# Optimization experiments

Measured on AMD Instinct MI355X. Metric: run time of the kernel, lower is better.

Reference implementation:

```python
import jax, jax.numpy as jnp
import numpy as np

NEG_SLOPE = 0.2  # PyG GATConv default leaky_relu negative_slope


def gat_conv(x, edge_index, W, att_src, att_dst, bias, heads, out_ch):
    """PyG GATConv (add_self_loops=False, concat=True, dropout disabled)."""
    N = x.shape[0]
    src, dst = edge_index[0], edge_index[1]
    h = (x @ W).reshape(N, heads, out_ch)               # [N,H,C]
    a_src = jnp.einsum('nhc,hc->nh', h, att_src)        # [N,H]
    a_dst = jnp.einsum('nhc,hc->nh', h, att_dst)        # [N,H]
    e = jax.nn.leaky_relu(a_src[src] + a_dst[dst], NEG_SLOPE)  # [E,H]
    # segment softmax over edges grouped by destination node
    e_max = jax.ops.segment_max(e, dst, num_segments=N)  # [N,H]
    e_exp = jnp.exp(e - e_max[dst])
    denom = jax.ops.segment_sum(e_exp, dst, num_segments=N)
    alpha = e_exp / (denom[dst] + 1e-16)                 # [E,H]
    msg = h[src] * alpha[:, :, None]                     # [E,H,C]
    out = jax.ops.segment_sum(msg, dst, num_segments=N)  # [N,H,C]
    return out.reshape(N, heads * out_ch) + bias


def setup_inputs() -> dict:
    key = jax.random.key(0)
    ks = jax.random.split(key, 10)
    N, E, F_IN, H, C1, OUT = 50000, 1600000, 256, 8, 8, 64
    s = 0.1
    return {
        'x': jax.random.normal(ks[0], (N, F_IN), jnp.float32),
        'edge_index': jax.random.randint(ks[1], (2, E), 0, N, jnp.int64),
        'W1': jax.random.normal(ks[2], (F_IN, H * C1), jnp.float32) * s,
        'att_src1': jax.random.normal(ks[3], (H, C1), jnp.float32) * s,
        'att_dst1': jax.random.normal(ks[4], (H, C1), jnp.float32) * s,
        'bias1': jax.random.normal(ks[5], (H * C1,), jnp.float32) * s,
        'W2': jax.random.normal(ks[6], (H * C1, OUT), jnp.float32) * s,
        'att_src2': jax.random.normal(ks[7], (1, OUT), jnp.float32) * s,
        'att_dst2': jax.random.normal(ks[8], (1, OUT), jnp.float32) * s,
        'bias2': jax.random.normal(ks[9], (OUT,), jnp.float32) * s,
    }


def reference(x, edge_index, W1, att_src1, att_dst1, bias1, W2, att_src2, att_dst2, bias2):
    # GAT.forward, eval mode with disable_dropout=True (no dropout, no loss)
    h = gat_conv(x, edge_index, W1, att_src1, att_dst1, bias1, heads=8, out_ch=8)
    h = jax.nn.elu(h)
    h = gat_conv(h, edge_index, W2, att_src2, att_dst2, bias2, heads=1, out_ch=64)
    return jax.nn.log_softmax(h, axis=1)
```

## Files before the change

### kernel.cpp

```cpp
#include <hip/hip_runtime.h>
#include <math.h>

#define LRELU 0.2f
#define BSH 7
#define BSZ (1 << BSH)
#define CH 8192
#define ECH 2048
#define GB 6

typedef __attribute__((ext_vector_type(8))) short bf16x8;
typedef __attribute__((ext_vector_type(4))) float f32x4;

static __device__ __forceinline__ float bf2f(unsigned int u16) {
    union { unsigned int i; float f; } c; c.i = u16 << 16; return c.f;
}
static __device__ __forceinline__ unsigned short f2bf(float f) {
    union { float f; unsigned int i; } c; c.f = f;
    unsigned int x = c.i;
    return (unsigned short)((x + 0x7fffu + ((x >> 16) & 1u)) >> 16);
}


__global__ __launch_bounds__(256) void k_bcount(const int* __restrict__ dst, int E,
                                                int NB, int* __restrict__ bcnt) {
    __shared__ int cnt[512];
    int t = threadIdx.x;
    for (int b = t; b < 512; b += 256) cnt[b] = 0;
    __syncthreads();
    int e0 = blockIdx.x * CH;
    int e1 = e0 + CH; if (e1 > E) e1 = E;
    for (int i = e0 + t; i < e1; i += 256) atomicAdd(&cnt[dst[i] >> BSH], 1);
    __syncthreads();
    for (int b = t; b < NB; b += 256) {
        int c = cnt[b];
        if (c) atomicAdd(&bcnt[b], c);
    }
}

__global__ __launch_bounds__(64) void k_bscan(const int* __restrict__ bcnt, int NB,
                                              int* __restrict__ boff,
                                              int* __restrict__ bcur) {
    int lane = threadIdx.x;
    int run = 0;
    for (int base = 0; base < NB; base += 64) {
        int v = (base + lane < NB) ? bcnt[base + lane] : 0;
        int inc = v;
#pragma unroll
        for (int off = 1; off < 64; off <<= 1) {
            int t = __shfl_up(inc, off, 64);
            if (lane >= off) inc += t;
        }
        if (base + lane < NB) {
            int e = run + inc - v;
            boff[base + lane] = e;
            bcur[base + lane] = e;
        }
        run += __shfl(inc, 63, 64);
    }
    if (lane == 0) boff[NB] = run;
}

__global__ __launch_bounds__(256) void k_binscat1(const int* __restrict__ src,
                                                  const int* __restrict__ dst,
                                                  int E, int NB,
                                                  int* __restrict__ bcur,
                                                  unsigned* __restrict__ pairs) {
    __shared__ int cnt[512];
    __shared__ int lds_d[CH];
    int t = threadIdx.x;
    int e0 = blockIdx.x * CH;
    int e1 = e0 + CH; if (e1 > E) e1 = E;
    int n = e1 - e0;
    for (int b = t; b < 512; b += 256) cnt[b] = 0;
    __syncthreads();
    for (int i = t; i < n; i += 256) {
        int d = dst[e0 + i];
        lds_d[i] = d;
        atomicAdd(&cnt[d >> BSH], 1);
    }
    __syncthreads();
    for (int b = t; b < NB; b += 256) {
        int c = cnt[b];
        cnt[b] = c ? atomicAdd(&bcur[b], c) : 0;
    }
    __syncthreads();
    for (int i = t; i < n; i += 256) {
        int d = lds_d[i];
        int p = atomicAdd(&cnt[d >> BSH], 1);
        pairs[p] = ((unsigned)src[e0 + i] << BSH) | (unsigned)(d & (BSZ - 1));
    }
}

__global__ __launch_bounds__(256) void k_bucket(const int* __restrict__ boff,
                                                const unsigned* __restrict__ pairs,
                                                int N, int* __restrict__ rowptr,
                                                int* __restrict__ col) {
    __shared__ int cnt[BSZ];
    __shared__ int cur[BSZ];
    int t = threadIdx.x;
    int b = blockIdx.x;
    int dlo = b << BSH;
    int dhi = dlo + BSZ; if (dhi > N) dhi = N;
    int nd = dhi - dlo;
    int jb = boff[b], je = boff[b + 1];
    if (t < BSZ) cnt[t] = 0;
    __syncthreads();
    for (int j = jb + t; j < je; j += 256) atomicAdd(&cnt[pairs[j] & (BSZ - 1)], 1);
    __syncthreads();
    if (t < 64) {
        int v0 = cnt[t], v1 = cnt[64 + t];
        int i0 = v0;
#pragma unroll
        for (int off = 1; off < 64; off <<= 1) {
            int q = __shfl_up(i0, off, 64);
            if (t >= off) i0 += q;
        }
        int tot0 = __shfl(i0, 63, 64);
        int i1 = v1;
#pragma unroll
        for (int off = 1; off < 64; off <<= 1) {
            int q = __shfl_up(i1, off, 64);
            if (t >= off) i1 += q;
        }
        int e0x = jb + i0 - v0;
        int e1x = jb + tot0 + i1 - v1;
        cur[t] = e0x;
        cur[64 + t] = e1x;
        if (t < nd) rowptr[dlo + t] = e0x;
        if (64 + t < nd) rowptr[dlo + 64 + t] = e1x;
        if (t == 0 && dhi == N) rowptr[N] = je;
    }
    __syncthreads();
    for (int j = jb + t; j < je; j += 256) {
        unsigned pk = pairs[j];
        int p = atomicAdd(&cur[pk & (BSZ - 1)], 1);
        col[p] = (int)(pk >> BSH);
    }
}

__global__ __launch_bounds__(256) void k_cvtW(const float* __restrict__ W1,
                                              const float* __restrict__ W2,
                                              unsigned short* __restrict__ Wt1,
                                              unsigned short* __restrict__ Wt2,
                                              float* __restrict__ s1,
                                              float* __restrict__ s2,
                                              unsigned short* __restrict__ h1b,
                                              unsigned short* __restrict__ gb,
                                              int N) {
    int idx = blockIdx.x * 256 + threadIdx.x;
    if (idx < 16384) {
        int n = idx >> 8, k = idx & 255;
        Wt1[idx] = f2bf(W1[k * 64 + n]);
    } else if (idx < 16384 + 4096) {
        int j = idx - 16384;
        int n = j >> 6, k = j & 63;
        Wt2[j] = f2bf(W2[k * 64 + n]);
    } else if (idx < 20488) {
        s1[(size_t)N * 8 + (idx - 20480)] = -1e30f;
    } else if (idx == 20488) {
        s2[N] = -1e30f;
    } else if (idx >= 20496 && idx < 20560) {
        h1b[(size_t)N * 64 + (idx - 20496)] = 0;
    } else if (idx >= 20560 && idx < 20624) {
        gb[(size_t)N * 64 + (idx - 20560)] = 0;
    }
}

__global__ __launch_bounds__(256) void k_gemm1m(const float* __restrict__ X,
                                                const unsigned short* __restrict__ Wt,
                                                const float* __restrict__ atts,
                                                const float* __restrict__ attd,
                                                int N, unsigned short* __restrict__ Hb,
                                                float* __restrict__ asrc,
                                                float* __restrict__ adst) {
    __shared__ short Xl[64 * 256];
    int t = threadIdx.x, l = t & 63, w = t >> 6;
    int rblk = blockIdx.x * 64;

    int half = l >> 5;
    int c8 = (l & 31) * 8;
#pragma unroll
    for (int i = 0; i < 8; ++i) {
        int rl = w * 16 + i * 2 + half;
        int row = rblk + rl;
        float4 x0 = {0.f, 0.f, 0.f, 0.f}, x1 = {0.f, 0.f, 0.f, 0.f};
        if (row < N) {
            x0 = *reinterpret_cast<const float4*>(X + (size_t)row * 256 + c8);
            x1 = *reinterpret_cast<const float4*>(X + (size_t)row * 256 + c8 + 4);
        }
        bf16x8 p;
        p[0] = (short)f2bf(x0.x); p[1] = (short)f2bf(x0.y);
        p[2] = (short)f2bf(x0.z); p[3] = (short)f2bf(x0.w);
        p[4] = (short)f2bf(x1.x); p[5] = (short)f2bf(x1.y);
        p[6] = (short)f2bf(x1.z); p[7] = (short)f2bf(x1.w);
        int g = (l & 31) ^ (rl & 7);
        *reinterpret_cast<bf16x8*>(&Xl[rl * 256 + g * 8]) = p;
    }

    int m = l & 15, quad = l >> 4;
    int rl = w * 16 + m;
    f32x4 acc0 = {0.f, 0.f, 0.f, 0.f}, acc1 = acc0, acc2 = acc0, acc3 = acc0;
#pragma unroll
    for (int tt = 0; tt < 8; ++tt) {
        int g = (tt * 4 + quad) ^ (m & 7);
        bf16x8 a = *reinterpret_cast<const bf16x8*>(&Xl[rl * 256 + g * 8]);
        int kk = tt * 32 + quad * 8;
        bf16x8 b0 = *reinterpret_cast<const bf16x8*>(&Wt[(0 * 16 + m) * 256 + kk]);
        bf16x8 b1 = *reinterpret_cast<const bf16x8*>(&Wt[(1 * 16 + m) * 256 + kk]);
        bf16x8 b2 = *reinterpret_cast<const bf16x8*>(&Wt[(2 * 16 + m) * 256 + kk]);
        bf16x8 b3 = *reinterpret_cast<const bf16x8*>(&Wt[(3 * 16 + m) * 256 + kk]);
        acc0 = __builtin_amdgcn_mfma_f32_16x16x32_bf16(a, b0, acc0, 0, 0, 0);
        acc1 = __builtin_amdgcn_mfma_f32_16x16x32_bf16(a, b1, acc1, 0, 0, 0);
        acc2 = __builtin_amdgcn_mfma_f32_16x16x32_bf16(a, b2, acc2, 0, 0, 0);
        acc3 = __builtin_amdgcn_mfma_f32_16x16x32_bf16(a, b3, acc3, 0, 0, 0);
    }

    int r0 = rblk + w * 16;
    f32x4 accs[4] = {acc0, acc1, acc2, acc3};
#pragma unroll
    for (int nt = 0; nt < 4; ++nt) {
        int cn = nt * 16 + m;
        float av_s = atts[cn], av_d = attd[cn];
#pragma unroll
        for (int r = 0; r < 4; ++r) {
            int row = r0 + quad * 4 + r;
            float hv = accs[nt][r];
            if (row < N) Hb[(size_t)row * 64 + cn] = f2bf(hv);
            float vs = hv * av_s, vd = hv * av_d;
            vs += __shfl_xor(vs, 1, 64); vs += __shfl_xor(vs, 2, 64); vs += __shfl_xor(vs, 4, 64);
            vd += __shfl_xor(vd, 1, 64); vd += __shfl_xor(vd, 2, 64); vd += __shfl_xor(vd, 4, 64);
            if ((m & 7) == 0 && row < N) {
                int head = cn >> 3;
                asrc[row * 8 + head] = vs;
                adst[row * 8 + head] = vd;
            }
        }
    }
}

__global__ __launch_bounds__(256) void k_gemm2m(const unsigned short* __restrict__ Xb,
                                                const unsigned short* __restrict__ Wt,
                                                const float* __restrict__ atts,
                                                const float* __restrict__ attd,
                                                int N, unsigned short* __restrict__ Gb,
                                                float* __restrict__ asrc,
                                                float* __restrict__ adst) {
    int t = threadIdx.x, l = t & 63, w = t >> 6;
    int rblk = blockIdx.x * 64;
    int m = l & 15, quad = l >> 4;
    int row = rblk + w * 16 + m;
    int rowc = (row < N) ? row : 0;

    f32x4 acc0 = {0.f, 0.f, 0.f, 0.f}, acc1 = acc0, acc2 = acc0, acc3 = acc0;
#pragma unroll
    for (int tt = 0; tt < 2; ++tt) {
        int kk = tt * 32 + quad * 8;
        bf16x8 a = *reinterpret_cast<const bf16x8*>(&Xb[(size_t)rowc * 64 + kk]);
        bf16x8 b0 = *reinterpret_cast<const bf16x8*>(&Wt[(0 * 16 + m) * 64 + kk]);
        bf16x8 b1 = *reinterpret_cast<const bf16x8*>(&Wt[(1 * 16 + m) * 64 + kk]);
        bf16x8 b2 = *reinterpret_cast<const bf16x8*>(&Wt[(2 * 16 + m) * 64 + kk]);
        bf16x8 b3 = *reinterpret_cast<const bf16x8*>(&Wt[(3 * 16 + m) * 64 + kk]);
        acc0 = __builtin_amdgcn_mfma_f32_16x16x32_bf16(a, b0, acc0, 0, 0, 0);
        acc1 = __builtin_amdgcn_mfma_f32_16x16x32_bf16(a, b1, acc1, 0, 0, 0);
        acc2 = __builtin_amdgcn_mfma_f32_16x16x32_bf16(a, b2, acc2, 0, 0, 0);
        acc3 = __builtin_amdgcn_mfma_f32_16x16x32_bf16(a, b3, acc3, 0, 0, 0);
    }

    int r0 = rblk + w * 16;
    f32x4 accs[4] = {acc0, acc1, acc2, acc3};
#pragma unroll
    for (int r = 0; r < 4; ++r) {
        int orow = r0 + quad * 4 + r;
        float vs = 0.f, vd = 0.f;
#pragma unroll
        for (int nt = 0; nt < 4; ++nt) {
            int cn = nt * 16 + m;
            float hv = accs[nt][r];
            if (orow < N) Gb[(size_t)orow * 64 + cn] = f2bf(hv);
            vs = fmaf(hv, atts[cn], vs);
            vd = fmaf(hv, attd[cn], vd);
        }
#pragma unroll
        for (int off = 1; off < 16; off <<= 1) {
            vs += __shfl_xor(vs, off, 64);
            vd += __shfl_xor(vd, off, 64);
        }
        if (m == 0 && orow < N) { asrc[orow] = vs; adst[orow] = vd; }
    }
}


__global__ __launch_bounds__(256) void k_gather1(const int* __restrict__ rowptr,
                                                 const int* __restrict__ col,
                                                 const uint4* __restrict__ Hb8,
                                                 const float* __restrict__ asrc,
                                                 const float* __restrict__ adst,
                                                 const float* __restrict__ bias,
                                                 int N,
                                                 unsigned short* __restrict__ outb) {
    __shared__ int colS[ECH];
    int t = threadIdx.x;
    int gid = t >> 3, sub = t & 7;
    int d0 = blockIdx.x * 32;
    int dend = d0 + 32; if (dend > N) dend = N;
    int d = d0 + gid;
    int dok = (d < dend);
    int dc = dok ? d : d0;
    int jb = rowptr[dc];
    int je = rowptr[dc + 1];
    if (!dok) { jb = 0; je = 0; }
    float adv = dok ? adst[dc * 8 + sub] : 0.f;
    int ebeg = rowptr[d0];
    int eend = rowptr[dend];

    float acc[8] = {0.f, 0.f, 0.f, 0.f, 0.f, 0.f, 0.f, 0.f};
    float denom = 0.f;
    for (int cb = ebeg; cb < eend; cb += ECH) {
        int ce = cb + ECH; if (ce > eend) ce = eend;
        int n = ce - cb;
        __syncthreads();
        for (int i = t; i < n; i += 256) colS[i] = col[cb + i];
        __syncthreads();
        int lo = (jb > cb) ? jb : cb;
        int hi = (je < ce) ? je : ce;
        for (int u = lo; u < hi; u += GB) {
            int s6[GB];
#pragma unroll
            for (int q = 0; q < GB; ++q) {
                int uu = u + q;
                s6[q] = (uu < hi) ? colS[uu - cb] : N;
            }
            float as6[GB];
#pragma unroll
            for (int q = 0; q < GB; ++q) as6[q] = asrc[s6[q] * 8 + sub];
            uint4 hv6[GB];
#pragma unroll
            for (int q = 0; q < GB; ++q) hv6[q] = Hb8[(size_t)s6[q] * 8 + sub];
            __builtin_amdgcn_sched_barrier(0);
#pragma unroll
            for (int q = 0; q < GB; ++q) {
                float e = as6[q] + adv;
                e = (e > 0.f) ? e : LRELU * e;
                float wgt = __expf(e);
                uint4 hv = hv6[q];
                denom += wgt;
                acc[0] = fmaf(wgt, bf2f(hv.x & 0xffffu), acc[0]);
                acc[1] = fmaf(wgt, bf2f(hv.x >> 16), acc[1]);
                acc[2] = fmaf(wgt, bf2f(hv.y & 0xffffu), acc[2]);
                acc[3] = fmaf(wgt, bf2f(hv.y >> 16), acc[3]);
                acc[4] = fmaf(wgt, bf2f(hv.z & 0xffffu), acc[4]);
                acc[5] = fmaf(wgt, bf2f(hv.z >> 16), acc[5]);
                acc[6] = fmaf(wgt, bf2f(hv.w & 0xffffu), acc[6]);
                acc[7] = fmaf(wgt, bf2f(hv.w >> 16), acc[7]);
            }
        }
    }
    if (dok) {
        float invd = 1.f / (denom + 1e-16f);
        unsigned short pk[8];
#pragma unroll
        for (int c = 0; c < 8; ++c) {
            float v = fmaf(acc[c], invd, bias[sub * 8 + c]);
            v = (v > 0.f) ? v : expm1f(v);
            pk[c] = f2bf(v);
        }
        uint4 pv;
        pv.x = (unsigned)pk[0] | ((unsigned)pk[1] << 16);
        pv.y = (unsigned)pk[2] | ((unsigned)pk[3] << 16);
        pv.z = (unsigned)pk[4] | ((unsigned)pk[5] << 16);
        pv.w = (unsigned)pk[6] | ((unsigned)pk[7] << 16);
        *reinterpret_cast<uint4*>(&outb[(size_t)d * 64 + sub * 8]) = pv;
    }
}

__global__ __launch_bounds__(256) void k_gather2(const int* __restrict__ rowptr,
                                                 const int* __restrict__ col,
                                                 const uint4* __restrict__ Gb8,
                                                 const float* __restrict__ asrc,
                                                 const float* __restrict__ adst,
                                                 const float* __restrict__ bias,
                                                 int N,
                                                 float* __restrict__ out) {
    __shared__ int colS[ECH];
    int t = threadIdx.x;
    int gid = t >> 3, sub = t & 7;
    int d0 = blockIdx.x * 32;
    int dend = d0 + 32; if (dend > N) dend = N;
    int d = d0 + gid;
    int dok = (d < dend);
    int dc = dok ? d : d0;
    int jb = rowptr[dc];
    int je = rowptr[dc + 1];
    if (!dok) { jb = 0; je = 0; }
    float adv = dok ? adst[dc] : 0.f;
    int ebeg = rowptr[d0];
    int eend = rowptr[dend];

    float acc[8] = {0.f, 0.f, 0.f, 0.f, 0.f, 0.f, 0.f, 0.f};
    float denom = 0.f;
    for (int cb = ebeg; cb < eend; cb += ECH) {
        int ce = cb + ECH; if (ce > eend) ce = eend;
        int n = ce - cb;
        __syncthreads();
        for (int i = t; i < n; i += 256) colS[i] = col[cb + i];
        __syncthreads();
        int lo = (jb > cb) ? jb : cb;
        int hi = (je < ce) ? je : ce;
        for (int u = lo; u < hi; u += GB) {
            int s6[GB];
#pragma unroll
            for (int q = 0; q < GB; ++q) {
                int uu = u + q;
                s6[q] = (uu < hi) ? colS[uu - cb] : N;
            }
            float as6[GB];
#pragma unroll
            for (int q = 0; q < GB; ++q) as6[q] = asrc[s6[q]];
            uint4 hv6[GB];
#pragma unroll
            for (int q = 0; q < GB; ++q) hv6[q] = Gb8[(size_t)s6[q] * 8 + sub];
            __builtin_amdgcn_sched_barrier(0);
#pragma unroll
            for (int q = 0; q < GB; ++q) {
                float e = as6[q] + adv;
                e = (e > 0.f) ? e : LRELU * e;
                float wgt = __expf(e);
                uint4 hv = hv6[q];
                denom += wgt;
                acc[0] = fmaf(wgt, bf2f(hv.x & 0xffffu), acc[0]);
                acc[1] = fmaf(wgt, bf2f(hv.x >> 16), acc[1]);
                acc[2] = fmaf(wgt, bf2f(hv.y & 0xffffu), acc[2]);
                acc[3] = fmaf(wgt, bf2f(hv.y >> 16), acc[3]);
                acc[4] = fmaf(wgt, bf2f(hv.z & 0xffffu), acc[4]);
                acc[5] = fmaf(wgt, bf2f(hv.z >> 16), acc[5]);
                acc[6] = fmaf(wgt, bf2f(hv.w & 0xffffu), acc[6]);
                acc[7] = fmaf(wgt, bf2f(hv.w >> 16), acc[7]);
            }
        }
    }
    float invd = 1.f / (denom + 1e-16f);
    float v[8];
#pragma unroll
    for (int c = 0; c < 8; ++c) v[c] = fmaf(acc[c], invd, bias[sub * 8 + c]);
    float m = v[0];
#pragma unroll
    for (int c = 1; c < 8; ++c) m = fmaxf(m, v[c]);
    m = fmaxf(m, __shfl_xor(m, 1, 64));
    m = fmaxf(m, __shfl_xor(m, 2, 64));
    m = fmaxf(m, __shfl_xor(m, 4, 64));
    float se = 0.f;
#pragma unroll
    for (int c = 0; c < 8; ++c) se += __expf(v[c] - m);
    se += __shfl_xor(se, 1, 64);
    se += __shfl_xor(se, 2, 64);
    se += __shfl_xor(se, 4, 64);
    float ls = m + __logf(se);
    if (dok) {
        float4 o0, o1;
        o0.x = v[0] - ls; o0.y = v[1] - ls; o0.z = v[2] - ls; o0.w = v[3] - ls;
        o1.x = v[4] - ls; o1.y = v[5] - ls; o1.z = v[6] - ls; o1.w = v[7] - ls;
        *reinterpret_cast<float4*>(&out[(size_t)d * 64 + sub * 8]) = o0;
        *reinterpret_cast<float4*>(&out[(size_t)d * 64 + sub * 8 + 4]) = o1;
    }
}


extern "C" void kernel_launch(void* const* d_in, const int* in_sizes, int n_in,
                              void* d_out, int out_size, void* d_ws, size_t ws_size,
                              hipStream_t stream) {
    const float* x   = (const float*)d_in[0];
    const int*   ei  = (const int*)d_in[1];
    const float* W1  = (const float*)d_in[2];
    const float* as1 = (const float*)d_in[3];
    const float* ad1 = (const float*)d_in[4];
    const float* b1  = (const float*)d_in[5];
    const float* W2  = (const float*)d_in[6];
    const float* as2 = (const float*)d_in[7];
    const float* ad2 = (const float*)d_in[8];
    const float* b2  = (const float*)d_in[9];
    float* out = (float*)d_out;

    const int N = in_sizes[0] / 256;
    const int E = in_sizes[1] / 2;
    const int* src = ei;
    const int* dst = ei + E;
    const int NB = (N + BSZ - 1) >> BSH;
    const int nchunk = (E + CH - 1) / CH;

    char* ws = (char*)d_ws;
    size_t off = 0;
    auto alloc = [&](size_t bytes) -> void* {
        void* p = ws + off;
        off = (off + bytes + 255) & ~(size_t)255;
        return p;
    };
    int*      bcnt   = (int*)alloc((size_t)NB * 4);
    int*      boff   = (int*)alloc((size_t)(NB + 1) * 4);
    int*      bcur   = (int*)alloc((size_t)NB * 4);
    int*      rowptr = (int*)alloc((size_t)(N + 1) * 4);
    int*      col    = (int*)alloc((size_t)E * 4);
    unsigned* pairs  = (unsigned*)alloc((size_t)E * 4);
    unsigned short* wt1 = (unsigned short*)alloc(64 * 256 * 2);
    unsigned short* wt2 = (unsigned short*)alloc(64 * 64 * 2);
    unsigned short* h1b = (unsigned short*)alloc((size_t)(N + 1) * 64 * 2);
    float* a_s1   = (float*)alloc(((size_t)N * 8 + 8) * 4);
    float* a_d1   = (float*)alloc((size_t)N * 8 * 4);
    unsigned short* h2b = (unsigned short*)alloc((size_t)N * 64 * 2);
    unsigned short* gb  = (unsigned short*)alloc((size_t)(N + 1) * 64 * 2);
    float* a_s2   = (float*)alloc((size_t)(N + 1) * 4);
    float* a_d2   = (float*)alloc((size_t)N * 4);
    (void)ws_size; (void)n_in; (void)out_size;

    k_cvtW<<<81, 256, 0, stream>>>(W1, W2, wt1, wt2, a_s1, a_s2, h1b, gb, N);

    hipMemsetAsync(bcnt, 0, (size_t)NB * 4, stream);
    k_bcount<<<nchunk, 256, 0, stream>>>(dst, E, NB, bcnt);
    k_bscan<<<1, 64, 0, stream>>>(bcnt, NB, boff, bcur);
    k_binscat1<<<nchunk, 256, 0, stream>>>(src, dst, E, NB, bcur, pairs);
    k_bucket<<<NB, 256, 0, stream>>>(boff, pairs, N, rowptr, col);

    int gblk = (N + 63) / 64;
    k_gemm1m<<<gblk, 256, 0, stream>>>(x, wt1, as1, ad1, N, h1b, a_s1, a_d1);

    int gather_blocks = (N + 31) / 32;
    k_gather1<<<gather_blocks, 256, 0, stream>>>(rowptr, col, (const uint4*)h1b,
                                                 a_s1, a_d1, b1, N, h2b);

    k_gemm2m<<<gblk, 256, 0, stream>>>(h2b, wt2, as2, ad2, N, gb, a_s2, a_d2);

    k_gather2<<<gather_blocks, 256, 0, stream>>>(rowptr, col, (const uint4*)gb,
                                                 a_s2, a_d2, b2, N, out);
}
```

Before: 249.9 us.

## Fuse layer-2 GEMM into layer-1 gather and merge prep kernels

Layer-2's linear projection now runs inside the layer-1 gather kernel. Each block stages its 32 ELU outputs in swizzled LDS and runs MFMA against the bf16 W2 to write the layer-2 features directly. The attention logits are computed from precomputed W2·att vectors in fp32 before bf16 rounding. The weight conversion and edge-bucket counting kernels are merged into one launch, and the gather batch size rises from 6 to 8 edges. This removes the h2b round trip and one launch, at the cost of more registers and a block-wide barrier in the gather kernel.

```diff
diff --git a/kernel.cpp b/kernel.cpp
--- a/kernel.cpp
+++ b/kernel.cpp
@@ -6,7 +6,7 @@
 #define BSZ (1 << BSH)
 #define CH 8192
 #define ECH 2048
-#define GB 6
+#define GB 8
 
 typedef __attribute__((ext_vector_type(8))) short bf16x8;
 typedef __attribute__((ext_vector_type(4))) float f32x4;
@@ -21,19 +21,64 @@
 }
 
 
-__global__ __launch_bounds__(256) void k_bcount(const int* __restrict__ dst, int E,
-                                                int NB, int* __restrict__ bcnt) {
+__global__ __launch_bounds__(256) void k_prep(const int* __restrict__ dst, int E,
+                                              int NB, int* __restrict__ bcnt,
+                                              const float* __restrict__ W1,
+                                              const float* __restrict__ W2,
+                                              const float* __restrict__ as2in,
+                                              const float* __restrict__ ad2in,
+                                              unsigned short* __restrict__ Wt1,
+                                              unsigned short* __restrict__ Wt2,
+                                              float* __restrict__ s1,
+                                              float* __restrict__ s2,
+                                              unsigned short* __restrict__ h1b,
+                                              unsigned short* __restrict__ gb,
+                                              float* __restrict__ w2s,
+                                              float* __restrict__ w2d,
+                                              int N, int nchunk) {
     __shared__ int cnt[512];
     int t = threadIdx.x;
-    for (int b = t; b < 512; b += 256) cnt[b] = 0;
-    __syncthreads();
-    int e0 = blockIdx.x * CH;
-    int e1 = e0 + CH; if (e1 > E) e1 = E;
-    for (int i = e0 + t; i < e1; i += 256) atomicAdd(&cnt[dst[i] >> BSH], 1);
-    __syncthreads();
-    for (int b = t; b < NB; b += 256) {
-        int c = cnt[b];
-        if (c) atomicAdd(&bcnt[b], c);
+    if ((int)blockIdx.x < nchunk) {
+        for (int b = t; b < 512; b += 256) cnt[b] = 0;
+        __syncthreads();
+        int e0 = blockIdx.x * CH;
+        int e1 = e0 + CH; if (e1 > E) e1 = E;
+        for (int i = e0 + t; i < e1; i += 256) atomicAdd(&cnt[dst[i] >> BSH], 1);
+        __syncthreads();
+        for (int b = t; b < NB; b += 256) {
+            int c = cnt[b];
+            if (c) atomicAdd(&bcnt[b], c);
+        }
+        return;
+    }
+    int idx = ((int)blockIdx.x - nchunk) * 256 + t;
+    if (idx < 16384) {
+        int n = idx >> 8, k = idx & 255;
+        Wt1[idx] = f2bf(W1[k * 64 + n]);
+    } else if (idx < 16384 + 4096) {
+        int j = idx - 16384;
+        int n = j >> 6, k = j & 63;
+        Wt2[j] = f2bf(W2[k * 64 + n]);
+    } else if (idx >= 20480 && idx < 20488) {
+        s1[(size_t)N * 8 + (idx - 20480)] = -1e30f;
+    } else if (idx == 20488) {
+        s2[N] = -1e30f;
+    } else if (idx >= 20496 && idx < 20560) {
+        h1b[(size_t)N * 64 + (idx - 20496)] = 0;
+    } else if (idx >= 20560 && idx < 20624) {
+        gb[(size_t)N * 64 + (idx - 20560)] = 0;
+    } else if (idx >= 20624 && idx < 20688) {
+        int c = idx - 20624;
+        float s = 0.f;
+#pragma unroll
+        for (int n = 0; n < 64; ++n) s += W2[c * 64 + n] * as2in[n];
+        w2s[c] = s;
+    } else if (idx >= 20688 && idx < 20752) {
+        int c = idx - 20688;
+        float s = 0.f;
+#pragma unroll
+        for (int n = 0; n < 64; ++n) s += W2[c * 64 + n] * ad2in[n];
+        w2d[c] = s;
     }
 }
 
@@ -138,34 +183,6 @@
     }
 }
 
-__global__ __launch_bounds__(256) void k_cvtW(const float* __restrict__ W1,
-                                              const float* __restrict__ W2,
-                                              unsigned short* __restrict__ Wt1,
-                                              unsigned short* __restrict__ Wt2,
-                                              float* __restrict__ s1,
-                                              float* __restrict__ s2,
-                                              unsigned short* __restrict__ h1b,
-                                              unsigned short* __restrict__ gb,
-                                              int N) {
-    int idx = blockIdx.x * 256 + threadIdx.x;
-    if (idx < 16384) {
-        int n = idx >> 8, k = idx & 255;
-        Wt1[idx] = f2bf(W1[k * 64 + n]);
-    } else if (idx < 16384 + 4096) {
-        int j = idx - 16384;
-        int n = j >> 6, k = j & 63;
-        Wt2[j] = f2bf(W2[k * 64 + n]);
-    } else if (idx < 20488) {
-        s1[(size_t)N * 8 + (idx - 20480)] = -1e30f;
-    } else if (idx == 20488) {
-        s2[N] = -1e30f;
-    } else if (idx >= 20496 && idx < 20560) {
-        h1b[(size_t)N * 64 + (idx - 20496)] = 0;
-    } else if (idx >= 20560 && idx < 20624) {
-        gb[(size_t)N * 64 + (idx - 20560)] = 0;
-    }
-}
-
 __global__ __launch_bounds__(256) void k_gemm1m(const float* __restrict__ X,
                                                 const unsigned short* __restrict__ Wt,
                                                 const float* __restrict__ atts,
@@ -238,67 +255,22 @@
     }
 }
 
-__global__ __launch_bounds__(256) void k_gemm2m(const unsigned short* __restrict__ Xb,
-                                                const unsigned short* __restrict__ Wt,
-                                                const float* __restrict__ atts,
-                                                const float* __restrict__ attd,
-                                                int N, unsigned short* __restrict__ Gb,
-                                                float* __restrict__ asrc,
-                                                float* __restrict__ adst) {
-    int t = threadIdx.x, l = t & 63, w = t >> 6;
-    int rblk = blockIdx.x * 64;
-    int m = l & 15, quad = l >> 4;
-    int row = rblk + w * 16 + m;
-    int rowc = (row < N) ? row : 0;
-
-    f32x4 acc0 = {0.f, 0.f, 0.f, 0.f}, acc1 = acc0, acc2 = acc0, acc3 = acc0;
-#pragma unroll
-    for (int tt = 0; tt < 2; ++tt) {
-        int kk = tt * 32 + quad * 8;
-        bf16x8 a = *reinterpret_cast<const bf16x8*>(&Xb[(size_t)rowc * 64 + kk]);
-        bf16x8 b0 = *reinterpret_cast<const bf16x8*>(&Wt[(0 * 16 + m) * 64 + kk]);
-        bf16x8 b1 = *reinterpret_cast<const bf16x8*>(&Wt[(1 * 16 + m) * 64 + kk]);
-        bf16x8 b2 = *reinterpret_cast<const bf16x8*>(&Wt[(2 * 16 + m) * 64 + kk]);
-        bf16x8 b3 = *reinterpret_cast<const bf16x8*>(&Wt[(3 * 16 + m) * 64 + kk]);
-        acc0 = __builtin_amdgcn_mfma_f32_16x16x32_bf16(a, b0, acc0, 0, 0, 0);
-        acc1 = __builtin_amdgcn_mfma_f32_16x16x32_bf16(a, b1, acc1, 0, 0, 0);
-        acc2 = __builtin_amdgcn_mfma_f32_16x16x32_bf16(a, b2, acc2, 0, 0, 0);
-        acc3 = __builtin_amdgcn_mfma_f32_16x16x32_bf16(a, b3, acc3, 0, 0, 0);
-    }
-
-    int r0 = rblk + w * 16;
-    f32x4 accs[4] = {acc0, acc1, acc2, acc3};
-#pragma unroll
-    for (int r = 0; r < 4; ++r) {
-        int orow = r0 + quad * 4 + r;
-        float vs = 0.f, vd = 0.f;
-#pragma unroll
-        for (int nt = 0; nt < 4; ++nt) {
-            int cn = nt * 16 + m;
-            float hv = accs[nt][r];
-            if (orow < N) Gb[(size_t)orow * 64 + cn] = f2bf(hv);
-            vs = fmaf(hv, atts[cn], vs);
-            vd = fmaf(hv, attd[cn], vd);
-        }
-#pragma unroll
-        for (int off = 1; off < 16; off <<= 1) {
-            vs += __shfl_xor(vs, off, 64);
-            vd += __shfl_xor(vd, off, 64);
-        }
-        if (m == 0 && orow < N) { asrc[orow] = vs; adst[orow] = vd; }
-    }
-}
-
-
-__global__ __launch_bounds__(256) void k_gather1(const int* __restrict__ rowptr,
-                                                 const int* __restrict__ col,
-                                                 const uint4* __restrict__ Hb8,
-                                                 const float* __restrict__ asrc,
-                                                 const float* __restrict__ adst,
-                                                 const float* __restrict__ bias,
-                                                 int N,
-                                                 unsigned short* __restrict__ outb) {
+
+__global__ __launch_bounds__(256) void k_gather1f(const int* __restrict__ rowptr,
+                                                  const int* __restrict__ col,
+                                                  const uint4* __restrict__ Hb8,
+                                                  const float* __restrict__ asrc,
+                                                  const float* __restrict__ adst,
+                                                  const float* __restrict__ bias,
+                                                  const unsigned short* __restrict__ Wt2,
+                                                  const float* __restrict__ w2s,
+                                                  const float* __restrict__ w2d,
+                                                  int N,
+                                                  unsigned short* __restrict__ Gb,
+                                                  float* __restrict__ as2,
+                                                  float* __restrict__ ad2) {
     __shared__ int colS[ECH];
+    __shared__ short h2l[32 * 64];
     int t = threadIdx.x;
     int gid = t >> 3, sub = t & 7;
     int d0 = blockIdx.x * 32;
@@ -324,25 +296,25 @@
         int lo = (jb > cb) ? jb : cb;
         int hi = (je < ce) ? je : ce;
         for (int u = lo; u < hi; u += GB) {
-            int s6[GB];
+            int s8[GB];
 #pragma unroll
             for (int q = 0; q < GB; ++q) {
                 int uu = u + q;
-                s6[q] = (uu < hi) ? colS[uu - cb] : N;
+                s8[q] = (uu < hi) ? colS[uu - cb] : N;
             }
-            float as6[GB];
-#pragma unroll
-            for (int q = 0; q < GB; ++q) as6[q] = asrc[s6[q] * 8 + sub];
-            uint4 hv6[GB];
-#pragma unroll
-            for (int q = 0; q < GB; ++q) hv6[q] = Hb8[(size_t)s6[q] * 8 + sub];
+            float as8[GB];
+#pragma unroll
+            for (int q = 0; q < GB; ++q) as8[q] = asrc[s8[q] * 8 + sub];
+            uint4 hv8[GB];
+#pragma unroll
+            for (int q = 0; q < GB; ++q) hv8[q] = Hb8[(size_t)s8[q] * 8 + sub];
             __builtin_amdgcn_sched_barrier(0);
 #pragma unroll
             for (int q = 0; q < GB; ++q) {
-                float e = as6[q] + adv;
+                float e = as8[q] + adv;
                 e = (e > 0.f) ? e : LRELU * e;
                 float wgt = __expf(e);
-                uint4 hv = hv6[q];
+                uint4 hv = hv8[q];
                 denom += wgt;
                 acc[0] = fmaf(wgt, bf2f(hv.x & 0xffffu), acc[0]);
                 acc[1] = fmaf(wgt, bf2f(hv.x >> 16), acc[1]);
@@ -355,21 +327,55 @@
             }
         }
     }
-    if (dok) {
-        float invd = 1.f / (denom + 1e-16f);
-        unsigned short pk[8];
-#pragma unroll
-        for (int c = 0; c < 8; ++c) {
-            float v = fmaf(acc[c], invd, bias[sub * 8 + c]);
-            v = (v > 0.f) ? v : expm1f(v);
-            pk[c] = f2bf(v);
-        }
-        uint4 pv;
-        pv.x = (unsigned)pk[0] | ((unsigned)pk[1] << 16);
-        pv.y = (unsigned)pk[2] | ((unsigned)pk[3] << 16);
-        pv.z = (unsigned)pk[4] | ((unsigned)pk[5] << 16);
-        pv.w = (unsigned)pk[6] | ((unsigned)pk[7] << 16);
-        *reinterpret_cast<uint4*>(&outb[(size_t)d * 64 + sub * 8]) = pv;
+
+    float invd = 1.f / (denom + 1e-16f);
+    float v[8];
+#pragma unroll
+    for (int c = 0; c < 8; ++c) {
+        float x = fmaf(acc[c], invd, bias[sub * 8 + c]);
+        v[c] = (x > 0.f) ? x : expm1f(x);
+    }
+    float vs = 0.f, vd = 0.f;
+#pragma unroll
+    for (int c = 0; c < 8; ++c) {
+        vs = fmaf(v[c], w2s[sub * 8 + c], vs);
+        vd = fmaf(v[c], w2d[sub * 8 + c], vd);
+    }
+    vs += __shfl_xor(vs, 1, 64); vs += __shfl_xor(vs, 2, 64); vs += __shfl_xor(vs, 4, 64);
+    vd += __shfl_xor(vd, 1, 64); vd += __shfl_xor(vd, 2, 64); vd += __shfl_xor(vd, 4, 64);
+    if (dok && sub == 0) { as2[d] = vs; ad2[d] = vd; }
+
+    bf16x8 p;
+#pragma unroll
+    for (int c = 0; c < 8; ++c) p[c] = (short)f2bf(v[c]);
+    *reinterpret_cast<bf16x8*>(&h2l[gid * 64 + (sub ^ (gid & 7)) * 8]) = p;
+    __syncthreads();
+
+    int l = t & 63, w = t >> 6;
+    int m = l & 15, quad = l >> 4;
+    int mt = w & 1;
+    int ntb = (w >> 1) * 2;
+    int r = mt * 16 + m;
+    f32x4 g0 = {0.f, 0.f, 0.f, 0.f}, g1 = g0;
+#pragma unroll
+    for (int tt = 0; tt < 2; ++tt) {
+        bf16x8 a = *reinterpret_cast<const bf16x8*>(
+            &h2l[r * 64 + ((tt * 4 + quad) ^ (r & 7)) * 8]);
+        int kk = tt * 32 + quad * 8;
+        bf16x8 b0 = *reinterpret_cast<const bf16x8*>(&Wt2[((ntb + 0) * 16 + m) * 64 + kk]);
+        bf16x8 b1 = *reinterpret_cast<const bf16x8*>(&Wt2[((ntb + 1) * 16 + m) * 64 + kk]);
+        g0 = __builtin_amdgcn_mfma_f32_16x16x32_bf16(a, b0, g0, 0, 0, 0);
+        g1 = __builtin_amdgcn_mfma_f32_16x16x32_bf16(a, b1, g1, 0, 0, 0);
+    }
+    f32x4 gs[2] = {g0, g1};
+#pragma unroll
+    for (int nt = 0; nt < 2; ++nt) {
+        int cn = (ntb + nt) * 16 + m;
+#pragma unroll
+        for (int rr = 0; rr < 4; ++rr) {
+            int dr = d0 + mt * 16 + quad * 4 + rr;
+            if (dr < N) Gb[(size_t)dr * 64 + cn] = f2bf(gs[nt][rr]);
+        }
     }
 }
 
@@ -407,25 +413,25 @@
         int lo = (jb > cb) ? jb : cb;
         int hi = (je < ce) ? je : ce;
         for (int u = lo; u < hi; u += GB) {
-            int s6[GB];
+            int s8[GB];
 #pragma unroll
             for (int q = 0; q < GB; ++q) {
                 int uu = u + q;
-                s6[q] = (uu < hi) ? colS[uu - cb] : N;
+                s8[q] = (uu < hi) ? colS[uu - cb] : N;
             }
-            float as6[GB];
-#pragma unroll
-            for (int q = 0; q < GB; ++q) as6[q] = asrc[s6[q]];
-            uint4 hv6[GB];
-#pragma unroll
-            for (int q = 0; q < GB; ++q) hv6[q] = Gb8[(size_t)s6[q] * 8 + sub];
+            float as8[GB];
+#pragma unroll
+            for (int q = 0; q < GB; ++q) as8[q] = asrc[s8[q]];
+            uint4 hv8[GB];
+#pragma unroll
+            for (int q = 0; q < GB; ++q) hv8[q] = Gb8[(size_t)s8[q] * 8 + sub];
             __builtin_amdgcn_sched_barrier(0);
 #pragma unroll
             for (int q = 0; q < GB; ++q) {
-                float e = as6[q] + adv;
+                float e = as8[q] + adv;
                 e = (e > 0.f) ? e : LRELU * e;
                 float wgt = __expf(e);
-                uint4 hv = hv6[q];
+                uint4 hv = hv8[q];
                 denom += wgt;
                 acc[0] = fmaf(wgt, bf2f(hv.x & 0xffffu), acc[0]);
                 acc[1] = fmaf(wgt, bf2f(hv.x >> 16), acc[1]);
@@ -505,16 +511,17 @@
     unsigned short* h1b = (unsigned short*)alloc((size_t)(N + 1) * 64 * 2);
     float* a_s1   = (float*)alloc(((size_t)N * 8 + 8) * 4);
     float* a_d1   = (float*)alloc((size_t)N * 8 * 4);
-    unsigned short* h2b = (unsigned short*)alloc((size_t)N * 64 * 2);
     unsigned short* gb  = (unsigned short*)alloc((size_t)(N + 1) * 64 * 2);
     float* a_s2   = (float*)alloc((size_t)(N + 1) * 4);
     float* a_d2   = (float*)alloc((size_t)N * 4);
+    float* w2s    = (float*)alloc(64 * 4);
+    float* w2d    = (float*)alloc(64 * 4);
     (void)ws_size; (void)n_in; (void)out_size;
 
-    k_cvtW<<<81, 256, 0, stream>>>(W1, W2, wt1, wt2, a_s1, a_s2, h1b, gb, N);
-
     hipMemsetAsync(bcnt, 0, (size_t)NB * 4, stream);
-    k_bcount<<<nchunk, 256, 0, stream>>>(dst, E, NB, bcnt);
+    k_prep<<<nchunk + 82, 256, 0, stream>>>(dst, E, NB, bcnt, W1, W2, as2, ad2,
+                                            wt1, wt2, a_s1, a_s2, h1b, gb,
+                                            w2s, w2d, N, nchunk);
     k_bscan<<<1, 64, 0, stream>>>(bcnt, NB, boff, bcur);
     k_binscat1<<<nchunk, 256, 0, stream>>>(src, dst, E, NB, bcur, pairs);
     k_bucket<<<NB, 256, 0, stream>>>(boff, pairs, N, rowptr, col);
@@ -523,10 +530,9 @@
     k_gemm1m<<<gblk, 256, 0, stream>>>(x, wt1, as1, ad1, N, h1b, a_s1, a_d1);
 
     int gather_blocks = (N + 31) / 32;
-    k_gather1<<<gather_blocks, 256, 0, stream>>>(rowptr, col, (const uint4*)h1b,
-                                                 a_s1, a_d1, b1, N, h2b);
-
-    k_gemm2m<<<gblk, 256, 0, stream>>>(h2b, wt2, as2, ad2, N, gb, a_s2, a_d2);
+    k_gather1f<<<gather_blocks, 256, 0, stream>>>(rowptr, col, (const uint4*)h1b,
+                                                  a_s1, a_d1, b1, wt2, w2s, w2d,
+                                                  N, gb, a_s2, a_d2);
 
     k_gather2<<<gather_blocks, 256, 0, stream>>>(rowptr, col, (const uint4*)gb,
                                                  a_s2, a_d2, b2, N, out);
```

New measurement: 247.7 us. About the same (-0.9%).
